# Optimization experiments

Hardware: AMD Instinct MI355X
Metric: run time of the kernel (lower is better)

Reference implementation:

```python
import jax, jax.numpy as jnp
import numpy as np

T, B, E, H = 1024, 8, 1024, 16
HD = E // H                       # 64
SCALE = float(HD * 1) ** -0.5     # scaling_factor = 1


def setup_inputs() -> dict:
    key = jax.random.key(0)
    ks = jax.random.split(key, 7)
    s = 0.02
    return {
        "query": jax.random.normal(ks[0], (T, B, E), jnp.float32),
        "key_padding_mask": jax.random.bernoulli(ks[1], 0.1, (B, T)),
        "attn_bias": jax.random.normal(ks[2], (1, H, T, T), jnp.float32) * 0.1,
        "wq": jax.random.normal(ks[3], (1, E, E), jnp.float32) * s,
        "wk": jax.random.normal(ks[4], (1, E, E), jnp.float32) * s,
        "wv": jax.random.normal(ks[5], (1, E, E), jnp.float32) * s,
        "wo": jax.random.normal(ks[6], (1, E, E), jnp.float32) * s,
    }


def _group_linear(x, w):
    # x: (T, B, nb*din), w: (nb, din, dout) -> (T, B, nb*dout). nb=1 here.
    t, b, _ = x.shape
    nb, din, dout = w.shape
    y = jnp.einsum('xnd,nde->xne', x.reshape(t * b, nb, din), w)
    return y.reshape(t, b, nb * dout)


def reference(query, key_padding_mask, attn_bias, wq, wk, wv, wo):
    q = _group_linear(query, wq) * SCALE
    k = _group_linear(query, wk)
    v = _group_linear(query, wv)

    # (T, B, E) -> (B*H, T, HD), matching torch view+transpose
    def split_heads(x):
        return x.reshape(T, B * H, HD).transpose(1, 0, 2)

    q, k, v = split_heads(q), split_heads(k), split_heads(v)

    scores = jnp.einsum('bth,bsh->bts', q, k).reshape(B, H, T, T)
    scores = scores + attn_bias
    scores = jnp.where(key_padding_mask[:, None, None, :], -jnp.inf, scores)
    probs = jax.nn.softmax(scores.astype(jnp.float32), axis=-1).astype(query.dtype)

    vh = v.reshape(B, H, T, HD)  # (B*H,T,HD) -> (B,H,S,HD)
    attn = jnp.einsum('bhts,bhsd->tbhd', probs, vh).reshape(T, B, H * HD)
    return _group_linear(attn, wo)
```

## Files before the change

kernel.cpp:

```cpp
#include <hip/hip_runtime.h>


typedef __bf16 bf16x8 __attribute__((ext_vector_type(8)));
typedef float f32x4 __attribute__((ext_vector_type(4)));

#define LOG2E 1.4426950408889634f
#define QSCALE 0.18033688011112042f

static __device__ __forceinline__ unsigned short f2bf_rn(float f) {
  union { float f; unsigned u; } x;
  x.f = f;
  unsigned r = (x.u + 0x7fffu + ((x.u >> 16) & 1u)) >> 16;
  return (unsigned short)r;
}
static __device__ __forceinline__ unsigned short f2bf(float f) {
  union { float f; unsigned u; } x;
  x.f = f;
  return (unsigned short)((x.u + 0x8000u) >> 16);
}

static __device__ __forceinline__ void async_cp16(const void* g, void* l) {
  __builtin_amdgcn_global_load_lds((__attribute__((address_space(1))) void*)g,
                                   (__attribute__((address_space(3))) void*)l,
                                   16, 0, 0);
}

__global__ void k_cvt(const float* __restrict__ src, unsigned short* __restrict__ dst) {
  const int idx = blockIdx.x * 256 + threadIdx.x;
  const float4 f = ((const float4*)src)[idx];
  unsigned lo = (unsigned)f2bf_rn(f.x) | ((unsigned)f2bf_rn(f.y) << 16);
  unsigned hi = (unsigned)f2bf_rn(f.z) | ((unsigned)f2bf_rn(f.w) << 16);
  uint2 v; v.x = lo; v.y = hi;
  *(uint2*)(dst + (size_t)idx * 4) = v;
}

__global__ void k_mask(const int* __restrict__ mask, float* __restrict__ Mfg) {
  const int i = blockIdx.x * 256 + threadIdx.x;
  Mfg[i] = mask[i] ? -1e30f : 0.f;
}

__global__ void k_transw(const float* __restrict__ src, unsigned short* __restrict__ dst) {
  __shared__ float tile[32][33];
  const int bx = blockIdx.x << 5;
  const int by = blockIdx.y << 5;
  const int tx = threadIdx.x, ty = threadIdx.y;
#pragma unroll
  for (int i = 0; i < 32; i += 8)
    tile[ty + i][tx] = src[(size_t)(by + ty + i) * 1024 + bx + tx];
  __syncthreads();
#pragma unroll
  for (int i = 0; i < 32; i += 8)
    dst[(size_t)(bx + ty + i) * 1024 + by + tx] = f2bf_rn(tile[tx][ty + i]);
}

__global__ __launch_bounds__(256, 2) void k_biasT(const float* __restrict__ bias,
                                                  unsigned short* __restrict__ B2) {
  __shared__ unsigned short tile[128 * 132];
  const int tid = threadIdx.x;
  const int ss = blockIdx.x, tt = blockIdx.y, h = blockIdx.z;
  const float* src = bias + ((long)h * 1024 + tt * 128) * 1024 + ss * 128;
#pragma unroll
  for (int c = 0; c < 16; ++c) {
    int flat = c * 256 + tid;
    int row = flat >> 5, col = (flat & 31) << 2;
    float4 v = *(const float4*)(src + (long)row * 1024 + col);
    unsigned short* t4 = &tile[row * 132 + col];
    t4[0] = f2bf_rn(v.x * LOG2E); t4[1] = f2bf_rn(v.y * LOG2E);
    t4[2] = f2bf_rn(v.z * LOG2E); t4[3] = f2bf_rn(v.w * LOG2E);
  }
  __syncthreads();
  const int wid = tid >> 6, lane = tid & 63, lanelo = lane & 15, quad = lane >> 4;
  unsigned short outv[64];
#pragma unroll
  for (int mi = 0; mi < 2; ++mi)
#pragma unroll
    for (int nj = 0; nj < 8; ++nj)
#pragma unroll
      for (int r = 0; r < 4; ++r)
        outv[mi * 32 + nj * 4 + r] =
            tile[(wid * 32 + mi * 16 + quad * 4 + r) * 132 + nj * 16 + lanelo];
  unsigned short* dst = B2 + ((((long)(h * 8 + tt) * 8 + ss) * 256 + tid) << 6);
#pragma unroll
  for (int i = 0; i < 8; ++i) ((uint4*)dst)[i] = ((const uint4*)outv)[i];
}

static __device__ __forceinline__ void gemm_tile_128x128(
    const unsigned short* __restrict__ A, const unsigned short* __restrict__ Bt,
    int K, long m0, long n0,
    unsigned short* As, unsigned short* Bs, f32x4 acc[4][4]) {
  const int tid = threadIdx.x;
  const int wid = tid >> 6;
  const int lane = tid & 63;
  const int lanelo = lane & 15;
  const int quad = lane >> 4;
  const int wm = (wid >> 1) << 6;
  const int wn = (wid & 1) << 6;
  const int srow = tid >> 2;
  const int scol = (tid & 3) << 3;

  for (int k0 = 0; k0 < K; k0 += 32) {
    __syncthreads();
    {
      const unsigned short* ga0 = A + (m0 + srow) * K + k0 + scol;
      const unsigned short* ga1 = A + (m0 + srow + 64) * K + k0 + scol;
      const unsigned short* gb0 = Bt + (n0 + srow) * K + k0 + scol;
      const unsigned short* gb1 = Bt + (n0 + srow + 64) * K + k0 + scol;
      char* la = (char*)As + wid * 1024;
      char* lb = (char*)Bs + wid * 1024;
      async_cp16(ga0, la);
      async_cp16(ga1, la + 4096);
      async_cp16(gb0, lb);
      async_cp16(gb1, lb + 4096);
    }
    __syncthreads();
    bf16x8 a[4], b[4];
#pragma unroll
    for (int i = 0; i < 4; ++i) {
      a[i] = *(const bf16x8*)(As + (wm + i * 16 + lanelo) * 32 + quad * 8);
      b[i] = *(const bf16x8*)(Bs + (wn + i * 16 + lanelo) * 32 + quad * 8);
    }
#pragma unroll
    for (int i = 0; i < 4; ++i)
#pragma unroll
      for (int j = 0; j < 4; ++j)
        acc[i][j] = __builtin_amdgcn_mfma_f32_16x16x32_bf16(a[i], b[j], acc[i][j], 0, 0, 0);
  }
}

__global__ __launch_bounds__(256, 2) void k_gemm_qkv(
    const unsigned short* __restrict__ A, const unsigned short* __restrict__ Bt,
    unsigned short* __restrict__ Qh, unsigned short* __restrict__ Kh,
    unsigned short* __restrict__ Vt) {
  __shared__ unsigned short smem[9216];
  unsigned short* As = smem;
  unsigned short* Bs = smem + 4096;
  f32x4 acc[4][4];
  const f32x4 z4 = {0.f, 0.f, 0.f, 0.f};
#pragma unroll
  for (int i = 0; i < 4; ++i)
#pragma unroll
    for (int j = 0; j < 4; ++j) acc[i][j] = z4;

  const long m0 = (long)blockIdx.y * 128;
  const long n0 = (long)blockIdx.x * 128;
  gemm_tile_128x128(A, Bt, 1024, m0, n0, As, Bs, acc);

  const int tid = threadIdx.x;
  const int wid = tid >> 6;
  const int lane = tid & 63;
  const int lanelo = lane & 15;
  const int quad = lane >> 4;
  const int wm = (wid >> 1) << 6;
  const int wn = (wid & 1) << 6;
  const int which = (int)(blockIdx.x >> 3);

  if (which == 2) {
    unsigned short* Vt_s = smem;
    const long t0g = m0 >> 3;
#pragma unroll
    for (int half = 0; half < 2; ++half) {
      __syncthreads();
      if ((wid & 1) == half) {
#pragma unroll
        for (int mi = 0; mi < 4; ++mi)
#pragma unroll
          for (int nj = 0; nj < 4; ++nj)
#pragma unroll
            for (int r = 0; r < 4; ++r)
              Vt_s[(wm + mi * 16 + quad * 4 + r) * 72 + nj * 16 + lanelo] =
                  f2bf(acc[mi][nj][r]);
      }
      __syncthreads();
      const int h = (((int)(n0 & 1023)) >> 6) + half;
#pragma unroll
      for (int pp = 0; pp < 2; ++pp) {
        int p = tid + pp * 256;
        int b = p >> 6, d = p & 63;
        long off = ((long)(b * 16 + h)) << 16;
        __attribute__((aligned(16))) unsigned short vals[16];
#pragma unroll
        for (int t = 0; t < 16; ++t) vals[t] = Vt_s[(t * 8 + b) * 72 + d];
        uint4* dst = (uint4*)(Vt + off + (long)d * 1024 + t0g);
        dst[0] = ((const uint4*)vals)[0];
        dst[1] = ((const uint4*)vals)[1];
      }
    }
  } else {
#pragma unroll
    for (int mi = 0; mi < 4; ++mi)
#pragma unroll
      for (int nj = 0; nj < 4; ++nj)
#pragma unroll
        for (int r = 0; r < 4; ++r) {
          int m = (int)m0 + wm + mi * 16 + quad * 4 + r;
          int n = (int)n0 + wn + nj * 16 + lanelo;
          float v = acc[mi][nj][r];
          int t = m >> 3, b = m & 7;
          int e = n & 1023, h = e >> 6, d = e & 63;
          long off = ((long)(b * 16 + h)) << 16;
          if (which == 0)
            Qh[off + t * 64 + d] = f2bf(v * QSCALE);
          else
            Kh[off + t * 64 + d] = f2bf(v);
        }
  }
}

__global__ __launch_bounds__(256, 2) void k_attn(
    const unsigned short* __restrict__ Qh, const unsigned short* __restrict__ Kh,
    const unsigned short* __restrict__ Vt, const unsigned short* __restrict__ B2,
    const float* __restrict__ Mfg, unsigned short* __restrict__ A2) {
  __shared__ unsigned short Ks[128 * 72];
  __shared__ unsigned short Vs[64 * 136];
  __shared__ unsigned short Ps[128 * 72];

  const int tid = threadIdx.x;
  const int wid = tid >> 6;
  const int lane = tid & 63;
  const int lanelo = lane & 15;
  const int quad = lane >> 4;
  const int bh = blockIdx.x;
  const int b = bh >> 4, h = bh & 15;
  const int tt = blockIdx.y;
  const int t0 = tt * 128;
  const long head = (long)bh << 16;

  bf16x8 aq[2][2];
#pragma unroll
  for (int mi = 0; mi < 2; ++mi)
#pragma unroll
    for (int ks = 0; ks < 2; ++ks)
      aq[mi][ks] = *(const bf16x8*)(Qh + head +
                                    (long)(t0 + wid * 32 + mi * 16 + lanelo) * 64 +
                                    ks * 32 + quad * 8);

  const f32x4 z4 = {0.f, 0.f, 0.f, 0.f};
  f32x4 Oacc[2][4];
#pragma unroll
  for (int mi = 0; mi < 2; ++mi)
#pragma unroll
    for (int dj = 0; dj < 4; ++dj) Oacc[mi][dj] = z4;
  float mrow[2][4], lrow[2][4];
#pragma unroll
  for (int mi = 0; mi < 2; ++mi)
#pragma unroll
    for (int r = 0; r < 4; ++r) { mrow[mi][r] = -1e30f; lrow[mi][r] = 0.f; }

  const long biasbase = (((long)(h * 8 + tt) * 8) * 256 + tid) << 6;

  for (int s0 = 0; s0 < 1024; s0 += 128) {
    bf16x8 bfr[8];
    {
      const bf16x8* bp8 = (const bf16x8*)(B2 + biasbase + ((long)(s0 >> 7) * 256 << 6));
#pragma unroll
      for (int i = 0; i < 8; ++i) bfr[i] = bp8[i];
    }
    float madd[8];
#pragma unroll
    for (int nj = 0; nj < 8; ++nj)
      madd[nj] = Mfg[(long)b * 1024 + s0 + nj * 16 + lanelo];

    __syncthreads();
#pragma unroll
    for (int c = 0; c < 4; ++c) {
      int flat = c * 2048 + tid * 8;
      int row = flat >> 6, col = flat & 63;
      uint4 v = *(const uint4*)(Kh + head + (long)(s0 + row) * 64 + col);
      *(uint4*)&Ks[row * 72 + col] = v;
    }
#pragma unroll
    for (int c = 0; c < 4; ++c) {
      int flat = c * 2048 + tid * 8;
      int row = flat >> 7, col = flat & 127;
      uint4 v = *(const uint4*)(Vt + head + (long)row * 1024 + s0 + col);
      *(uint4*)&Vs[row * 136 + col] = v;
    }
    __syncthreads();

    f32x4 S[2][8];
#pragma unroll
    for (int mi = 0; mi < 2; ++mi)
#pragma unroll
      for (int nj = 0; nj < 8; ++nj) S[mi][nj] = z4;
#pragma unroll
    for (int ks = 0; ks < 2; ++ks) {
      bf16x8 bk[8];
#pragma unroll
      for (int nj = 0; nj < 8; ++nj)
        bk[nj] = *(const bf16x8*)(Ks + (nj * 16 + lanelo) * 72 + ks * 32 + quad * 8);
#pragma unroll
      for (int mi = 0; mi < 2; ++mi)
#pragma unroll
        for (int nj = 0; nj < 8; ++nj)
          S[mi][nj] = __builtin_amdgcn_mfma_f32_16x16x32_bf16(aq[mi][ks], bk[nj], S[mi][nj], 0, 0, 0);
    }

#pragma unroll
    for (int mi = 0; mi < 2; ++mi)
#pragma unroll
      for (int nj = 0; nj < 8; ++nj)
#pragma unroll
        for (int r = 0; r < 4; ++r)
          S[mi][nj][r] += (float)bfr[mi * 4 + (nj >> 1)][(nj & 1) * 4 + r] + madd[nj];

#pragma unroll
    for (int mi = 0; mi < 2; ++mi)
#pragma unroll
      for (int r = 0; r < 4; ++r) {
        float mx = -1e30f;
#pragma unroll
        for (int nj = 0; nj < 8; ++nj) mx = fmaxf(mx, S[mi][nj][r]);
        mx = fmaxf(mx, __shfl_xor(mx, 1, 16));
        mx = fmaxf(mx, __shfl_xor(mx, 2, 16));
        mx = fmaxf(mx, __shfl_xor(mx, 4, 16));
        mx = fmaxf(mx, __shfl_xor(mx, 8, 16));
        float mold = mrow[mi][r];
        float mnew = fmaxf(mold, mx);
        float al = exp2f(mold - mnew);
        mrow[mi][r] = mnew;
        float rs = 0.f;
#pragma unroll
        for (int nj = 0; nj < 8; ++nj) {
          float p = exp2f(S[mi][nj][r] - mnew);
          S[mi][nj][r] = p;
          rs += p;
        }
        rs += __shfl_xor(rs, 1, 16);
        rs += __shfl_xor(rs, 2, 16);
        rs += __shfl_xor(rs, 4, 16);
        rs += __shfl_xor(rs, 8, 16);
        lrow[mi][r] = lrow[mi][r] * al + rs;
#pragma unroll
        for (int dj = 0; dj < 4; ++dj) Oacc[mi][dj][r] *= al;
      }

#pragma unroll
    for (int half = 0; half < 2; ++half) {
#pragma unroll
      for (int mi = 0; mi < 2; ++mi)
#pragma unroll
        for (int njl = 0; njl < 4; ++njl)
#pragma unroll
          for (int r = 0; r < 4; ++r)
            Ps[(wid * 32 + mi * 16 + quad * 4 + r) * 72 + njl * 16 + lanelo] =
                f2bf(S[mi][half * 4 + njl][r]);
#pragma unroll
      for (int ks2 = 0; ks2 < 2; ++ks2) {
        const int ks = half * 2 + ks2;
        bf16x8 ap[2], bv[4];
#pragma unroll
        for (int mi = 0; mi < 2; ++mi)
          ap[mi] = *(const bf16x8*)(Ps + (wid * 32 + mi * 16 + lanelo) * 72 + ks2 * 32 + quad * 8);
#pragma unroll
        for (int dj = 0; dj < 4; ++dj)
          bv[dj] = *(const bf16x8*)(Vs + (dj * 16 + lanelo) * 136 + ks * 32 + quad * 8);
#pragma unroll
        for (int mi = 0; mi < 2; ++mi)
#pragma unroll
          for (int dj = 0; dj < 4; ++dj)
            Oacc[mi][dj] = __builtin_amdgcn_mfma_f32_16x16x32_bf16(ap[mi], bv[dj], Oacc[mi][dj], 0, 0, 0);
      }
    }
  }

#pragma unroll
  for (int mi = 0; mi < 2; ++mi)
#pragma unroll
    for (int r = 0; r < 4; ++r) {
      float rinv = __builtin_amdgcn_rcpf(lrow[mi][r]);
      int t = t0 + wid * 32 + mi * 16 + quad * 4 + r;
#pragma unroll
      for (int dj = 0; dj < 4; ++dj) {
        int d = dj * 16 + lanelo;
        A2[(long)(t * 8 + b) * 1024 + h * 64 + d] = f2bf(Oacc[mi][dj][r] * rinv);
      }
    }
}

__global__ __launch_bounds__(256, 2) void k_gemm_out(
    const unsigned short* __restrict__ A, const unsigned short* __restrict__ Bt,
    float* __restrict__ out) {
  __shared__ unsigned short As[128 * 32];
  __shared__ unsigned short Bs[128 * 32];
  f32x4 acc[4][4];
  const f32x4 z4 = {0.f, 0.f, 0.f, 0.f};
#pragma unroll
  for (int i = 0; i < 4; ++i)
#pragma unroll
    for (int j = 0; j < 4; ++j) acc[i][j] = z4;

  const long m0 = (long)blockIdx.y * 128;
  const long n0 = (long)blockIdx.x * 128;
  gemm_tile_128x128(A, Bt, 1024, m0, n0, As, Bs, acc);

  const int tid = threadIdx.x;
  const int wid = tid >> 6;
  const int lane = tid & 63;
  const int lanelo = lane & 15;
  const int quad = lane >> 4;
  const int wm = (wid >> 1) << 6;
  const int wn = (wid & 1) << 6;
#pragma unroll
  for (int mi = 0; mi < 4; ++mi)
#pragma unroll
    for (int nj = 0; nj < 4; ++nj)
#pragma unroll
      for (int r = 0; r < 4; ++r) {
        long m = m0 + wm + mi * 16 + quad * 4 + r;
        long n = n0 + wn + nj * 16 + lanelo;
        out[m * 1024 + n] = acc[mi][nj][r];
      }
}

extern "C" void kernel_launch(void* const* d_in, const int* in_sizes, int n_in,
                              void* d_out, int out_size, void* d_ws, size_t ws_size,
                              hipStream_t stream) {
  const float* query = (const float*)d_in[0];
  const int* mask = (const int*)d_in[1];
  const float* bias = (const float*)d_in[2];
  const float* wq = (const float*)d_in[3];
  const float* wk = (const float*)d_in[4];
  const float* wv = (const float*)d_in[5];
  const float* wo = (const float*)d_in[6];
  float* out = (float*)d_out;

  char* ws = (char*)d_ws;
  const size_t MB = 1024 * 1024;
  unsigned short* Abuf  = (unsigned short*)(ws);
  unsigned short* WqkvT = (unsigned short*)(ws + 16 * MB);
  unsigned short* WoT   = (unsigned short*)(ws + 22 * MB);
  unsigned short* Qh    = (unsigned short*)(ws + 24 * MB);
  unsigned short* Kh    = (unsigned short*)(ws + 40 * MB);
  unsigned short* Vt    = (unsigned short*)(ws + 56 * MB);
  unsigned short* A2    = (unsigned short*)(ws + 72 * MB);
  unsigned short* B2    = (unsigned short*)(ws + 88 * MB);
  float*          Mfg   = (float*)(ws + 120 * MB);

  k_cvt<<<dim3(8192), dim3(256), 0, stream>>>(query, Abuf);
  k_mask<<<dim3(32), dim3(256), 0, stream>>>(mask, Mfg);
  dim3 tb(32, 8);
  k_transw<<<dim3(32, 32), tb, 0, stream>>>(wq, WqkvT);
  k_transw<<<dim3(32, 32), tb, 0, stream>>>(wk, WqkvT + 1024 * 1024);
  k_transw<<<dim3(32, 32), tb, 0, stream>>>(wv, WqkvT + 2 * 1024 * 1024);
  k_transw<<<dim3(32, 32), tb, 0, stream>>>(wo, WoT);
  k_biasT<<<dim3(8, 8, 16), dim3(256), 0, stream>>>(bias, B2);
  k_gemm_qkv<<<dim3(24, 64), dim3(256), 0, stream>>>(Abuf, WqkvT, Qh, Kh, Vt);
  k_attn<<<dim3(128, 8), dim3(256), 0, stream>>>(Qh, Kh, Vt, B2, Mfg, A2);
  k_gemm_out<<<dim3(8, 64), dim3(256), 0, stream>>>(A2, WoT, out);
}
```

Measured before the change: 393.2 us.

## Split attention block across 8 waves with 16 query rows each

The attention kernel now launches 512 threads per block, and each of 8 waves owns 16 query rows instead of 32. This halves per-wave register state (S, Oacc, bias fragments), and the launch bound is raised to ask for more resident waves. Bias and mask are now loaded straight into the score accumulator before the QK MFMA instead of being added afterwards. In exchange, each wave reloads the same K/V fragments from LDS for half as much work, so LDS read traffic per FLOP rises. The bias indexing also has to match the k_biasT layout exactly.

Measured after the change: 381.8 us. -2.9%, faster.

```diff
diff --git a/kernel.cpp b/kernel.cpp
--- a/kernel.cpp
+++ b/kernel.cpp
@@ -206,7 +206,7 @@
   }
 }
 
-__global__ __launch_bounds__(256, 2) void k_attn(
+__global__ __launch_bounds__(512, 4) void k_attn(
     const unsigned short* __restrict__ Qh, const unsigned short* __restrict__ Kh,
     const unsigned short* __restrict__ Vt, const unsigned short* __restrict__ B2,
     const float* __restrict__ Mfg, unsigned short* __restrict__ A2) {
@@ -225,35 +225,30 @@
   const int t0 = tt * 128;
   const long head = (long)bh << 16;
 
-  bf16x8 aq[2][2];
-#pragma unroll
-  for (int mi = 0; mi < 2; ++mi)
-#pragma unroll
-    for (int ks = 0; ks < 2; ++ks)
-      aq[mi][ks] = *(const bf16x8*)(Qh + head +
-                                    (long)(t0 + wid * 32 + mi * 16 + lanelo) * 64 +
-                                    ks * 32 + quad * 8);
+  bf16x8 aq[2];
+#pragma unroll
+  for (int ks = 0; ks < 2; ++ks)
+    aq[ks] = *(const bf16x8*)(Qh + head +
+                              (long)(t0 + wid * 16 + lanelo) * 64 +
+                              ks * 32 + quad * 8);
 
   const f32x4 z4 = {0.f, 0.f, 0.f, 0.f};
-  f32x4 Oacc[2][4];
-#pragma unroll
-  for (int mi = 0; mi < 2; ++mi)
-#pragma unroll
-    for (int dj = 0; dj < 4; ++dj) Oacc[mi][dj] = z4;
-  float mrow[2][4], lrow[2][4];
-#pragma unroll
-  for (int mi = 0; mi < 2; ++mi)
-#pragma unroll
-    for (int r = 0; r < 4; ++r) { mrow[mi][r] = -1e30f; lrow[mi][r] = 0.f; }
-
-  const long biasbase = (((long)(h * 8 + tt) * 8) * 256 + tid) << 6;
+  f32x4 Oacc[4];
+#pragma unroll
+  for (int dj = 0; dj < 4; ++dj) Oacc[dj] = z4;
+  float mrow[4], lrow[4];
+#pragma unroll
+  for (int r = 0; r < 4; ++r) { mrow[r] = -1e30f; lrow[r] = 0.f; }
+
+  const long biasbase = (((long)(h * 8 + tt) * 8) * 256 + (wid >> 1) * 64 + lane) * 64 +
+                        (wid & 1) * 32;
 
   for (int s0 = 0; s0 < 1024; s0 += 128) {
-    bf16x8 bfr[8];
+    bf16x8 bfr[4];
     {
       const bf16x8* bp8 = (const bf16x8*)(B2 + biasbase + ((long)(s0 >> 7) * 256 << 6));
 #pragma unroll
-      for (int i = 0; i < 8; ++i) bfr[i] = bp8[i];
+      for (int i = 0; i < 4; ++i) bfr[i] = bp8[i];
     }
     float madd[8];
 #pragma unroll
@@ -262,26 +257,28 @@
 
     __syncthreads();
 #pragma unroll
-    for (int c = 0; c < 4; ++c) {
-      int flat = c * 2048 + tid * 8;
+    for (int c = 0; c < 2; ++c) {
+      int flat = c * 4096 + tid * 8;
       int row = flat >> 6, col = flat & 63;
       uint4 v = *(const uint4*)(Kh + head + (long)(s0 + row) * 64 + col);
       *(uint4*)&Ks[row * 72 + col] = v;
     }
 #pragma unroll
-    for (int c = 0; c < 4; ++c) {
-      int flat = c * 2048 + tid * 8;
+    for (int c = 0; c < 2; ++c) {
+      int flat = c * 4096 + tid * 8;
       int row = flat >> 7, col = flat & 127;
       uint4 v = *(const uint4*)(Vt + head + (long)row * 1024 + s0 + col);
       *(uint4*)&Vs[row * 136 + col] = v;
     }
     __syncthreads();
 
-    f32x4 S[2][8];
-#pragma unroll
-    for (int mi = 0; mi < 2; ++mi)
-#pragma unroll
-      for (int nj = 0; nj < 8; ++nj) S[mi][nj] = z4;
+    f32x4 S[8];
+#pragma unroll
+    for (int nj = 0; nj < 8; ++nj)
+#pragma unroll
+      for (int r = 0; r < 4; ++r)
+        S[nj][r] = (float)bfr[nj >> 1][(nj & 1) * 4 + r] + madd[nj];
+
 #pragma unroll
     for (int ks = 0; ks < 2; ++ks) {
       bf16x8 bk[8];
@@ -289,92 +286,72 @@
       for (int nj = 0; nj < 8; ++nj)
         bk[nj] = *(const bf16x8*)(Ks + (nj * 16 + lanelo) * 72 + ks * 32 + quad * 8);
 #pragma unroll
-      for (int mi = 0; mi < 2; ++mi)
-#pragma unroll
-        for (int nj = 0; nj < 8; ++nj)
-          S[mi][nj] = __builtin_amdgcn_mfma_f32_16x16x32_bf16(aq[mi][ks], bk[nj], S[mi][nj], 0, 0, 0);
-    }
-
-#pragma unroll
-    for (int mi = 0; mi < 2; ++mi)
-#pragma unroll
       for (int nj = 0; nj < 8; ++nj)
+        S[nj] = __builtin_amdgcn_mfma_f32_16x16x32_bf16(aq[ks], bk[nj], S[nj], 0, 0, 0);
+    }
+
+#pragma unroll
+    for (int r = 0; r < 4; ++r) {
+      float mx = S[0][r];
+#pragma unroll
+      for (int nj = 1; nj < 8; ++nj) mx = fmaxf(mx, S[nj][r]);
+      mx = fmaxf(mx, __shfl_xor(mx, 1, 16));
+      mx = fmaxf(mx, __shfl_xor(mx, 2, 16));
+      mx = fmaxf(mx, __shfl_xor(mx, 4, 16));
+      mx = fmaxf(mx, __shfl_xor(mx, 8, 16));
+      float mold = mrow[r];
+      float mnew = fmaxf(mold, mx);
+      float al = exp2f(mold - mnew);
+      mrow[r] = mnew;
+      float rs = 0.f;
+#pragma unroll
+      for (int nj = 0; nj < 8; ++nj) {
+        float p = exp2f(S[nj][r] - mnew);
+        S[nj][r] = p;
+        rs += p;
+      }
+      rs += __shfl_xor(rs, 1, 16);
+      rs += __shfl_xor(rs, 2, 16);
+      rs += __shfl_xor(rs, 4, 16);
+      rs += __shfl_xor(rs, 8, 16);
+      lrow[r] = lrow[r] * al + rs;
+#pragma unroll
+      for (int dj = 0; dj < 4; ++dj) Oacc[dj][r] *= al;
+    }
+
+#pragma unroll
+    for (int half = 0; half < 2; ++half) {
+#pragma unroll
+      for (int njl = 0; njl < 4; ++njl)
 #pragma unroll
         for (int r = 0; r < 4; ++r)
-          S[mi][nj][r] += (float)bfr[mi * 4 + (nj >> 1)][(nj & 1) * 4 + r] + madd[nj];
-
-#pragma unroll
-    for (int mi = 0; mi < 2; ++mi)
-#pragma unroll
-      for (int r = 0; r < 4; ++r) {
-        float mx = -1e30f;
-#pragma unroll
-        for (int nj = 0; nj < 8; ++nj) mx = fmaxf(mx, S[mi][nj][r]);
-        mx = fmaxf(mx, __shfl_xor(mx, 1, 16));
-        mx = fmaxf(mx, __shfl_xor(mx, 2, 16));
-        mx = fmaxf(mx, __shfl_xor(mx, 4, 16));
-        mx = fmaxf(mx, __shfl_xor(mx, 8, 16));
-        float mold = mrow[mi][r];
-        float mnew = fmaxf(mold, mx);
-        float al = exp2f(mold - mnew);
-        mrow[mi][r] = mnew;
-        float rs = 0.f;
-#pragma unroll
-        for (int nj = 0; nj < 8; ++nj) {
-          float p = exp2f(S[mi][nj][r] - mnew);
-          S[mi][nj][r] = p;
-          rs += p;
-        }
-        rs += __shfl_xor(rs, 1, 16);
-        rs += __shfl_xor(rs, 2, 16);
-        rs += __shfl_xor(rs, 4, 16);
-        rs += __shfl_xor(rs, 8, 16);
-        lrow[mi][r] = lrow[mi][r] * al + rs;
-#pragma unroll
-        for (int dj = 0; dj < 4; ++dj) Oacc[mi][dj][r] *= al;
-      }
-
-#pragma unroll
-    for (int half = 0; half < 2; ++half) {
-#pragma unroll
-      for (int mi = 0; mi < 2; ++mi)
-#pragma unroll
-        for (int njl = 0; njl < 4; ++njl)
-#pragma unroll
-          for (int r = 0; r < 4; ++r)
-            Ps[(wid * 32 + mi * 16 + quad * 4 + r) * 72 + njl * 16 + lanelo] =
-                f2bf(S[mi][half * 4 + njl][r]);
+          Ps[(wid * 16 + quad * 4 + r) * 72 + njl * 16 + lanelo] =
+              f2bf(S[half * 4 + njl][r]);
 #pragma unroll
       for (int ks2 = 0; ks2 < 2; ++ks2) {
         const int ks = half * 2 + ks2;
-        bf16x8 ap[2], bv[4];
-#pragma unroll
-        for (int mi = 0; mi < 2; ++mi)
-          ap[mi] = *(const bf16x8*)(Ps + (wid * 32 + mi * 16 + lanelo) * 72 + ks2 * 32 + quad * 8);
+        bf16x8 ap, bv[4];
+        ap = *(const bf16x8*)(Ps + (wid * 16 + lanelo) * 72 + ks2 * 32 + quad * 8);
 #pragma unroll
         for (int dj = 0; dj < 4; ++dj)
           bv[dj] = *(const bf16x8*)(Vs + (dj * 16 + lanelo) * 136 + ks * 32 + quad * 8);
 #pragma unroll
-        for (int mi = 0; mi < 2; ++mi)
-#pragma unroll
-          for (int dj = 0; dj < 4; ++dj)
-            Oacc[mi][dj] = __builtin_amdgcn_mfma_f32_16x16x32_bf16(ap[mi], bv[dj], Oacc[mi][dj], 0, 0, 0);
+        for (int dj = 0; dj < 4; ++dj)
+          Oacc[dj] = __builtin_amdgcn_mfma_f32_16x16x32_bf16(ap, bv[dj], Oacc[dj], 0, 0, 0);
       }
     }
   }
 
 #pragma unroll
-  for (int mi = 0; mi < 2; ++mi)
-#pragma unroll
-    for (int r = 0; r < 4; ++r) {
-      float rinv = __builtin_amdgcn_rcpf(lrow[mi][r]);
-      int t = t0 + wid * 32 + mi * 16 + quad * 4 + r;
-#pragma unroll
-      for (int dj = 0; dj < 4; ++dj) {
-        int d = dj * 16 + lanelo;
-        A2[(long)(t * 8 + b) * 1024 + h * 64 + d] = f2bf(Oacc[mi][dj][r] * rinv);
-      }
-    }
+  for (int r = 0; r < 4; ++r) {
+    float rinv = __builtin_amdgcn_rcpf(lrow[r]);
+    int t = t0 + wid * 16 + quad * 4 + r;
+#pragma unroll
+    for (int dj = 0; dj < 4; ++dj) {
+      int d = dj * 16 + lanelo;
+      A2[(long)(t * 8 + b) * 1024 + h * 64 + d] = f2bf(Oacc[dj][r] * rinv);
+    }
+  }
 }
 
 __global__ __launch_bounds__(256, 2) void k_gemm_out(
@@ -445,6 +422,6 @@
   k_transw<<<dim3(32, 32), tb, 0, stream>>>(wo, WoT);
   k_biasT<<<dim3(8, 8, 16), dim3(256), 0, stream>>>(bias, B2);
   k_gemm_qkv<<<dim3(24, 64), dim3(256), 0, stream>>>(Abuf, WqkvT, Qh, Kh, Vt);
-  k_attn<<<dim3(128, 8), dim3(256), 0, stream>>>(Qh, Kh, Vt, B2, Mfg, A2);
+  k_attn<<<dim3(128, 8), dim3(512), 0, stream>>>(Qh, Kh, Vt, B2, Mfg, A2);
   k_gemm_out<<<dim3(8, 64), dim3(256), 0, stream>>>(A2, WoT, out);
 }
```
